# Performance work log

Measured on AMD Instinct MI355X. Metric: run time of the kernel, lower is better.

The kernel has to match this reference:

```python
import jax, jax.numpy as jnp
import numpy as np

BLOCK = 32  # GGUF Q8_0 block size: one scale per 32 int8 quants


def setup_inputs() -> dict:
    key = jax.random.key(0)
    k1, k2, k3, k4 = jax.random.split(key, 4)
    B, S, D_IN, D_OUT = 2, 2048, 4096, 16384
    x = jax.random.normal(k1, (B, S, D_IN), dtype=jnp.float32)
    # Stored quantized weights: unsigned byte codes in [0,255]; dequant as (q-128)*scale
    weight_q = jax.random.randint(k2, (D_OUT, D_IN), 0, 255, dtype=jnp.int32)
    # One positive scale per 32-element block along in_features
    scales = jax.random.uniform(k3, (D_OUT, D_IN // BLOCK), dtype=jnp.float32) * 0.02 + 1e-3
    bias = jax.random.normal(k4, (D_OUT,), dtype=jnp.float32)
    return {"x": x, "weight_q": weight_q, "scales": scales, "bias": bias}


def _dequant(weight_q, scales):
    # weight_q: [O, I] int codes, scales: [O, I/BLOCK] -> fp weight [O, I]
    O, I = weight_q.shape
    q = (weight_q.astype(jnp.float32) - 128.0).reshape(O, I // BLOCK, BLOCK)
    return (q * scales[:, :, None]).reshape(O, I)


def reference(x, weight_q, scales, bias):
    # Fused dequant + matmul: y = x @ dequant(W).T + bias
    w = _dequant(weight_q, scales)  # [O, I]
    y = jnp.einsum("bsi,oi->bso", x, w)
    return y + bias
```

## Files before the change

kernel.cpp:

```cpp
#include <hip/hip_runtime.h>
#include <hip/hip_bf16.h>

typedef __attribute__((ext_vector_type(8))) short short8;
typedef __attribute__((ext_vector_type(4))) float f32x4;

#define AS1 __attribute__((address_space(1)))
#define AS3 __attribute__((address_space(3)))

static __device__ __forceinline__ short f2bf(float f) {
    __hip_bfloat16 h = __float2bfloat16(f);
    union { __hip_bfloat16 h; short s; } u;
    u.h = h;
    return u.s;
}


__global__ __launch_bounds__(256) void prepack_w_kernel(const int* __restrict__ wq,
                                                        const float* __restrict__ scales,
                                                        short* __restrict__ Wb,
                                                        long total8) {
    long i = (long)blockIdx.x * 256 + threadIdx.x;
    if (i >= total8) return;
    const int4* p = (const int4*)wq + i * 2;
    int4 q0 = p[0], q1 = p[1];
    float s = scales[(i * 8) >> 5];
    short8 v;
    v[0] = f2bf((float)(q0.x - 128) * s);
    v[1] = f2bf((float)(q0.y - 128) * s);
    v[2] = f2bf((float)(q0.z - 128) * s);
    v[3] = f2bf((float)(q0.w - 128) * s);
    v[4] = f2bf((float)(q1.x - 128) * s);
    v[5] = f2bf((float)(q1.y - 128) * s);
    v[6] = f2bf((float)(q1.z - 128) * s);
    v[7] = f2bf((float)(q1.w - 128) * s);
    ((short8*)Wb)[i] = v;
}

__global__ __launch_bounds__(256) void prepack_x_kernel(const float* __restrict__ x,
                                                        short* __restrict__ Xb,
                                                        long total8) {
    long i = (long)blockIdx.x * 256 + threadIdx.x;
    if (i >= total8) return;
    const float4* p = (const float4*)x + i * 2;
    float4 f0 = p[0], f1 = p[1];
    short8 v;
    v[0] = f2bf(f0.x); v[1] = f2bf(f0.y); v[2] = f2bf(f0.z); v[3] = f2bf(f0.w);
    v[4] = f2bf(f1.x); v[5] = f2bf(f1.y); v[6] = f2bf(f1.z); v[7] = f2bf(f1.w);
    ((short8*)Xb)[i] = v;
}

__global__ __launch_bounds__(512, 2)
void gemm256_kernel(const float* __restrict__ bias,
                    const short* __restrict__ Xb, const short* __restrict__ Wb,
                    float* __restrict__ out, int M, int N, int K) {
    __shared__ alignas(16) short As[4 * 8192];
    __shared__ alignas(16) short Bs[4 * 8192];

    const int nM = M >> 8, nN = N >> 8;
    int bid = blockIdx.x;
    {
        int nwg = nM * nN;
        if ((nwg & 7) == 0) bid = (bid & 7) * (nwg >> 3) + (bid >> 3);
    }
    int pm, pn;
    {
        const int G = 8;
        if ((nN % G) == 0) {
            int per = nM * G;
            int grp = bid / per, in = bid % per;
            pn = grp * G + (in % G);
            pm = in / G;
        } else { pn = bid % nN; pm = bid / nN; }
    }

    const int tid  = threadIdx.x;
    const int lane = tid & 63;
    const int wid  = tid >> 6;
    const int wm   = wid >> 2;
    const int wn   = wid & 3;
    const int q4   = lane >> 4;
    const int l15  = lane & 15;
    const int lx   = lane & 7;

    const long bm = (long)pm << 8, bn = (long)pn << 8;
    const long Kl = K;
    const int  NT = K >> 6;

    int rdA[2], rdB[2];
#pragma unroll
    for (int p = 0; p < 2; ++p) {
        rdA[p] = (p * 2 + wm) * 8192 + l15 * 64;
        rdB[p] = (p * 2 + (wn >> 1)) * 8192 + ((wn & 1) * 64 + l15) * 64;
    }
    const int sg0 = ((0 * 4 + q4) ^ lx) * 8;
    const int sg1 = ((1 * 4 + q4) ^ lx) * 8;

    const int chnk    = wid * 1024;
    const int srowrel = wid * 16 + (lane >> 3);
    const int scol    = ((lane & 7) ^ (lane >> 3)) * 8;

    const short* aSrc[2][2];
    const short* bSrc[2][2];
#pragma unroll
    for (int H = 0; H < 2; ++H)
#pragma unroll
        for (int j = 0; j < 2; ++j) {
            aSrc[H][j] = Xb + (bm + H * 128 + srowrel + j * 8) * Kl + scol;
            bSrc[H][j] = Wb + (bn + H * 128 + srowrel + j * 8) * Kl + scol;
        }

#define STAGE_A(H, t1) { int p_ = (t1) & 1; long ko_ = (long)(t1) << 6;              \
    __builtin_amdgcn_global_load_lds((const AS1 void*)(aSrc[H][0] + ko_),            \
        (AS3 void*)&As[(p_ * 2 + (H)) * 8192 + chnk], 16, 0, 0);                     \
    __builtin_amdgcn_global_load_lds((const AS1 void*)(aSrc[H][1] + ko_),            \
        (AS3 void*)&As[(p_ * 2 + (H)) * 8192 + chnk + 512], 16, 0, 0); }
#define STAGE_B(H, t2) { int p_ = (t2) & 1; long ko_ = (long)(t2) << 6;              \
    __builtin_amdgcn_global_load_lds((const AS1 void*)(bSrc[H][0] + ko_),            \
        (AS3 void*)&Bs[(p_ * 2 + (H)) * 8192 + chnk], 16, 0, 0);                     \
    __builtin_amdgcn_global_load_lds((const AS1 void*)(bSrc[H][1] + ko_),            \
        (AS3 void*)&Bs[(p_ * 2 + (H)) * 8192 + chnk + 512], 16, 0, 0); }

    f32x4 acc[8][4];
#pragma unroll
    for (int m = 0; m < 8; ++m)
#pragma unroll
        for (int n = 0; n < 4; ++n) acc[m][n] = (f32x4){0.f, 0.f, 0.f, 0.f};

    short8 bfr[4][2];

    STAGE_B(0, 0); STAGE_B(1, 0);
    STAGE_A(0, 0); STAGE_A(1, 0);
    if (NT > 1) {
        STAGE_B(0, 1); STAGE_B(1, 1);
        asm volatile("s_waitcnt vmcnt(4)" ::: "memory");
    } else {
        asm volatile("s_waitcnt vmcnt(0)" ::: "memory");
    }
    __builtin_amdgcn_s_barrier();

    for (int t = 0; t < NT; ++t) {
        const int par = t & 1;
        const int ra = rdA[par], rb = rdB[par];
        const bool s1 = (t + 1 < NT), s2 = (t + 2 < NT);

#pragma unroll
        for (int q = 0; q < 4; ++q) {
            short8 ak[2][2];
#pragma unroll
            for (int mi = 0; mi < 2; ++mi) {
                ak[mi][0] = *(const short8*)&As[ra + (2 * q + mi) * 1024 + sg0];
                ak[mi][1] = *(const short8*)&As[ra + (2 * q + mi) * 1024 + sg1];
            }
            if (q == 0) {
#pragma unroll
                for (int n = 0; n < 4; ++n) {
                    bfr[n][0] = *(const short8*)&Bs[rb + n * 1024 + sg0];
                    bfr[n][1] = *(const short8*)&Bs[rb + n * 1024 + sg1];
                }
            }
            if (q == 0) { if (s1) STAGE_A(0, t + 1); }
            else if (q == 1) { if (s1) STAGE_A(1, t + 1); }
            else if (q == 2) { if (s2) STAGE_B(0, t + 2); }
            else           { if (s2) STAGE_B(1, t + 2); }

            if (q == 0) asm volatile("s_waitcnt lgkmcnt(8)" ::: "memory");
            __builtin_amdgcn_s_barrier();
            asm volatile("s_waitcnt lgkmcnt(0)" ::: "memory");
            __builtin_amdgcn_sched_barrier(0);

            __builtin_amdgcn_s_setprio(1);
#pragma unroll
            for (int mi = 0; mi < 2; ++mi) {
#pragma unroll
                for (int n = 0; n < 4; ++n)
                    acc[2 * q + mi][n] = __builtin_amdgcn_mfma_f32_16x16x32_bf16(
                        ak[mi][0], bfr[n][0], acc[2 * q + mi][n], 0, 0, 0);
#pragma unroll
                for (int n = 0; n < 4; ++n)
                    acc[2 * q + mi][n] = __builtin_amdgcn_mfma_f32_16x16x32_bf16(
                        ak[mi][1], bfr[n][1], acc[2 * q + mi][n], 0, 0, 0);
            }
            __builtin_amdgcn_s_setprio(0);

            if (q == 3) {
                if (s2)      asm volatile("s_waitcnt vmcnt(4)" ::: "memory");
                else if (s1) asm volatile("s_waitcnt vmcnt(0)" ::: "memory");
            }
            __builtin_amdgcn_s_barrier();
        }
        __builtin_amdgcn_sched_barrier(0);
    }

#pragma unroll
    for (int n = 0; n < 4; ++n) {
        long col = bn + wn * 64 + n * 16 + l15;
        float bv = bias[col];
#pragma unroll
        for (int m = 0; m < 8; ++m) {
            long row = bm + wm * 128 + m * 16 + q4 * 4;
#pragma unroll
            for (int r = 0; r < 4; ++r)
                out[(row + r) * (long)N + col] = acc[m][n][r] + bv;
        }
    }
#undef STAGE_A
#undef STAGE_B
}


template <bool PRE_A, bool PRE_B>
__global__ __launch_bounds__(256, 2)
void gemm_kernel(const float* __restrict__ x, const int* __restrict__ wq,
                 const float* __restrict__ scales, const float* __restrict__ bias,
                 const short* __restrict__ Xb, const short* __restrict__ Wb,
                 float* __restrict__ out, int M, int N, int K) {
    constexpr int BM = 128, BN = 128, BK = 64;
    __shared__ alignas(16) short As[BM * BK];
    __shared__ alignas(16) short Bs[BN * BK];

    const int nM = M / BM, nN = N / BN;
    int bid = blockIdx.x;
    int pm, pn;
    const int G = 8;
    if ((nN % G) == 0) {
        int per = nM * G;
        int grp = bid / per;
        int in  = bid % per;
        pn = grp * G + (in % G);
        pm = in / G;
    } else {
        pn = bid % nN;
        pm = bid / nN;
    }

    const int tid  = threadIdx.x;
    const int lane = tid & 63;
    const int wv   = tid >> 6;
    const int wm   = (wv >> 1) * 64;
    const int wn   = (wv & 1) * 64;
    const int q    = lane >> 4;
    const int l15  = lane & 15;
    const int sxor = lane & 7;

    const long bm = (long)pm * BM, bn = (long)pn * BN;

    f32x4 acc[4][4];
#pragma unroll
    for (int i = 0; i < 4; ++i)
#pragma unroll
        for (int j = 0; j < 4; ++j) acc[i][j] = (f32x4){0.f, 0.f, 0.f, 0.f};

    const int srow = tid >> 3;
    const int scg  = tid & 7;

    const int sg0   = q ^ sxor;
    const int aOff0 = (wm + l15) * 64 + sg0 * 8;
    const int aOff1 = (wm + l15) * 64 + (sg0 ^ 4) * 8;
    const int bOff0 = (wn + l15) * 64 + sg0 * 8;
    const int bOff1 = (wn + l15) * 64 + (sg0 ^ 4) * 8;

    const int prRow  = lane >> 3;
    const int prGsrc = (lane & 7) ^ (lane >> 3);

    for (int k0 = 0; k0 < K; k0 += BK) {
        if constexpr (PRE_A) {
#pragma unroll
            for (int i = 0; i < 4; ++i) {
                int r = wv * 32 + i * 8 + prRow;
                const short* src = Xb + (bm + r) * (long)K + k0 + prGsrc * 8;
                __builtin_amdgcn_global_load_lds((const AS1 void*)src,
                                                 (AS3 void*)&As[(wv * 32 + i * 8) * 64],
                                                 16, 0, 0);
            }
        } else {
#pragma unroll
            for (int i = 0; i < 4; ++i) {
                int r = i * 32 + srow;
                const float4* p = (const float4*)(x + (bm + r) * (long)K + k0 + scg * 8);
                float4 f0 = p[0], f1 = p[1];
                short8 v;
                v[0] = f2bf(f0.x); v[1] = f2bf(f0.y); v[2] = f2bf(f0.z); v[3] = f2bf(f0.w);
                v[4] = f2bf(f1.x); v[5] = f2bf(f1.y); v[6] = f2bf(f1.z); v[7] = f2bf(f1.w);
                int sg = scg ^ (r & 7);
                *(short8*)&As[r * 64 + sg * 8] = v;
            }
        }
        if constexpr (PRE_B) {
#pragma unroll
            for (int i = 0; i < 4; ++i) {
                int r = wv * 32 + i * 8 + prRow;
                const short* src = Wb + (bn + r) * (long)K + k0 + prGsrc * 8;
                __builtin_amdgcn_global_load_lds((const AS1 void*)src,
                                                 (AS3 void*)&Bs[(wv * 32 + i * 8) * 64],
                                                 16, 0, 0);
            }
        } else {
#pragma unroll
            for (int i = 0; i < 4; ++i) {
                int r = i * 32 + srow;
                const int4* p = (const int4*)(wq + (bn + r) * (long)K + k0 + scg * 8);
                int4 q0 = p[0], q1 = p[1];
                float s = scales[(bn + r) * (long)(K >> 5) + ((k0 + scg * 8) >> 5)];
                short8 v;
                v[0] = f2bf((float)(q0.x - 128) * s);
                v[1] = f2bf((float)(q0.y - 128) * s);
                v[2] = f2bf((float)(q0.z - 128) * s);
                v[3] = f2bf((float)(q0.w - 128) * s);
                v[4] = f2bf((float)(q1.x - 128) * s);
                v[5] = f2bf((float)(q1.y - 128) * s);
                v[6] = f2bf((float)(q1.z - 128) * s);
                v[7] = f2bf((float)(q1.w - 128) * s);
                int sg = scg ^ (r & 7);
                *(short8*)&Bs[r * 64 + sg * 8] = v;
            }
        }
        __syncthreads();

#pragma unroll
        for (int kk = 0; kk < 2; ++kk) {
            short8 a[4], b[4];
            const int aBase = kk ? aOff1 : aOff0;
            const int bBase = kk ? bOff1 : bOff0;
#pragma unroll
            for (int mi = 0; mi < 4; ++mi) a[mi] = *(const short8*)&As[aBase + mi * 16 * 64];
#pragma unroll
            for (int nj = 0; nj < 4; ++nj) b[nj] = *(const short8*)&Bs[bBase + nj * 16 * 64];
#pragma unroll
            for (int mi = 0; mi < 4; ++mi)
#pragma unroll
                for (int nj = 0; nj < 4; ++nj)
                    acc[mi][nj] = __builtin_amdgcn_mfma_f32_16x16x32_bf16(
                        a[mi], b[nj], acc[mi][nj], 0, 0, 0);
        }
        __syncthreads();
    }

#pragma unroll
    for (int nj = 0; nj < 4; ++nj) {
        long col = bn + wn + nj * 16 + l15;
        float bv = bias[col];
#pragma unroll
        for (int mi = 0; mi < 4; ++mi) {
            long row = bm + wm + mi * 16 + q * 4;
#pragma unroll
            for (int r2 = 0; r2 < 4; ++r2)
                out[(row + r2) * (long)N + col] = acc[mi][nj][r2] + bv;
        }
    }
}


extern "C" void kernel_launch(void* const* d_in, const int* in_sizes, int n_in,
                              void* d_out, int out_size, void* d_ws, size_t ws_size,
                              hipStream_t stream) {
    const float* x      = (const float*)d_in[0];
    const int*   wq     = (const int*)d_in[1];
    const float* scales = (const float*)d_in[2];
    const float* bias   = (const float*)d_in[3];
    float*       out    = (float*)d_out;

    const long N = (long)in_sizes[3];
    const long K = (long)in_sizes[1] / N;
    const long M = (long)in_sizes[0] / K;

    const size_t needW = (size_t)N * K * sizeof(short);
    const size_t needX = (size_t)M * K * sizeof(short);

    short* Wb = (short*)d_ws;
    short* Xb = Wb + (size_t)N * K;

    const bool preB = (d_ws != nullptr) && ws_size >= needW;
    const bool preA = preB && ws_size >= (needW + needX);

    if (preB) {
        long t8 = N * K / 8;
        prepack_w_kernel<<<dim3((unsigned)((t8 + 255) / 256)), dim3(256), 0, stream>>>(
            wq, scales, Wb, t8);
    }
    if (preA) {
        long t8 = M * K / 8;
        prepack_x_kernel<<<dim3((unsigned)((t8 + 255) / 256)), dim3(256), 0, stream>>>(
            x, Xb, t8);
    }

    const bool big = preA && (M % 256 == 0) && (N % 256 == 0) && (K % 64 == 0) && (K / 64 >= 2);

    if (big) {
        dim3 grid((unsigned)((M / 256) * (N / 256))), block(512);
        gemm256_kernel<<<grid, block, 0, stream>>>(bias, Xb, Wb, out, (int)M, (int)N, (int)K);
    } else {
        dim3 grid((unsigned)((M / 128) * (N / 128))), block(256);
        if (preA)
            gemm_kernel<true, true><<<grid, block, 0, stream>>>(x, wq, scales, bias, Xb, Wb,
                                                                out, (int)M, (int)N, (int)K);
        else if (preB)
            gemm_kernel<false, true><<<grid, block, 0, stream>>>(x, wq, scales, bias, Xb, Wb,
                                                                 out, (int)M, (int)N, (int)K);
        else
            gemm_kernel<false, false><<<grid, block, 0, stream>>>(x, wq, scales, bias, Xb, Wb,
                                                                  out, (int)M, (int)N, (int)K);
    }
}
```

Measured before the change: 645.1 us.

## Software-pipeline LDS fragment reads with ping-pong registers across MFMA phases

Restructures the main K loop of the 256x256 GEMM so that A fragments for the next phase are read from LDS into alternate register buffers (akP/akQ) while the current phase's MFMAs run. Next-tile B fragments are interleaved with the last MFMA phase. The last iteration is peeled into an epilogue. The aim is to hide LDS read latency behind matrix math and cut the full lgkmcnt(0) waits per phase, at the cost of more registers and a fragile hand-written wait schedule. It also drops the NT==1 guard in the prologue.

```diff
diff --git a/kernel.cpp b/kernel.cpp
--- a/kernel.cpp
+++ b/kernel.cpp
@@ -92,8 +92,8 @@
         rdA[p] = (p * 2 + wm) * 8192 + l15 * 64;
         rdB[p] = (p * 2 + (wn >> 1)) * 8192 + ((wn & 1) * 64 + l15) * 64;
     }
-    const int sg0 = ((0 * 4 + q4) ^ lx) * 8;
-    const int sg1 = ((1 * 4 + q4) ^ lx) * 8;
+    const int sg0 = (q4 ^ lx) * 8;
+    const int sg1 = ((4 + q4) ^ lx) * 8;
 
     const int chnk    = wid * 1024;
     const int srowrel = wid * 16 + (lane >> 3);
@@ -120,75 +120,122 @@
     __builtin_amdgcn_global_load_lds((const AS1 void*)(bSrc[H][1] + ko_),            \
         (AS3 void*)&Bs[(p_ * 2 + (H)) * 8192 + chnk + 512], 16, 0, 0); }
 
+#define LDA4(BUF, mbase, ra_) {                                                      \
+    BUF[0][0] = *(const short8*)&As[(ra_) + (mbase) * 1024 + sg0];                   \
+    BUF[0][1] = *(const short8*)&As[(ra_) + (mbase) * 1024 + sg1];                   \
+    BUF[1][0] = *(const short8*)&As[(ra_) + ((mbase) + 1) * 1024 + sg0];             \
+    BUF[1][1] = *(const short8*)&As[(ra_) + ((mbase) + 1) * 1024 + sg1]; }
+
+#define LGKM4  asm volatile("s_waitcnt lgkmcnt(4)" ::: "memory");                    \
+               __builtin_amdgcn_sched_barrier(0)
+#define LGKM0  asm volatile("s_waitcnt lgkmcnt(0)" ::: "memory");                    \
+               __builtin_amdgcn_sched_barrier(0)
+
+#define MFMA_PH(row0, A) {                                                           \
+    __builtin_amdgcn_s_setprio(1);                                                   \
+    _Pragma("unroll")                                                                \
+    for (int n = 0; n < 4; ++n)                                                      \
+        acc[row0][n] = __builtin_amdgcn_mfma_f32_16x16x32_bf16(A[0][0], bfr[n][0],   \
+                                                               acc[row0][n], 0,0,0); \
+    _Pragma("unroll")                                                                \
+    for (int n = 0; n < 4; ++n)                                                      \
+        acc[row0][n] = __builtin_amdgcn_mfma_f32_16x16x32_bf16(A[0][1], bfr[n][1],   \
+                                                               acc[row0][n], 0,0,0); \
+    _Pragma("unroll")                                                                \
+    for (int n = 0; n < 4; ++n)                                                      \
+        acc[(row0)+1][n] = __builtin_amdgcn_mfma_f32_16x16x32_bf16(A[1][0],          \
+                                           bfr[n][0], acc[(row0)+1][n], 0,0,0);      \
+    _Pragma("unroll")                                                                \
+    for (int n = 0; n < 4; ++n)                                                      \
+        acc[(row0)+1][n] = __builtin_amdgcn_mfma_f32_16x16x32_bf16(A[1][1],          \
+                                           bfr[n][1], acc[(row0)+1][n], 0,0,0);      \
+    __builtin_amdgcn_s_setprio(0); }
+
     f32x4 acc[8][4];
 #pragma unroll
     for (int m = 0; m < 8; ++m)
 #pragma unroll
         for (int n = 0; n < 4; ++n) acc[m][n] = (f32x4){0.f, 0.f, 0.f, 0.f};
 
-    short8 bfr[4][2];
-
-    STAGE_B(0, 0); STAGE_B(1, 0);
-    STAGE_A(0, 0); STAGE_A(1, 0);
-    if (NT > 1) {
-        STAGE_B(0, 1); STAGE_B(1, 1);
-        asm volatile("s_waitcnt vmcnt(4)" ::: "memory");
-    } else {
-        asm volatile("s_waitcnt vmcnt(0)" ::: "memory");
-    }
+    short8 akP[2][2], akQ[2][2], bfr[4][2];
+
+    STAGE_B(0, 0); STAGE_B(1, 0); STAGE_A(0, 0); STAGE_A(1, 0);
+    STAGE_B(0, 1); STAGE_B(1, 1);
+    asm volatile("s_waitcnt vmcnt(4)" ::: "memory");
     __builtin_amdgcn_s_barrier();
-
-    for (int t = 0; t < NT; ++t) {
+    LDA4(akP, 0, rdA[0]);
+#pragma unroll
+    for (int n = 0; n < 4; ++n) {
+        bfr[n][0] = *(const short8*)&Bs[rdB[0] + n * 1024 + sg0];
+        bfr[n][1] = *(const short8*)&Bs[rdB[0] + n * 1024 + sg1];
+    }
+
+    for (int t = 0; t < NT - 1; ++t) {
         const int par = t & 1;
-        const int ra = rdA[par], rb = rdB[par];
-        const bool s1 = (t + 1 < NT), s2 = (t + 2 < NT);
-
-#pragma unroll
-        for (int q = 0; q < 4; ++q) {
-            short8 ak[2][2];
-#pragma unroll
-            for (int mi = 0; mi < 2; ++mi) {
-                ak[mi][0] = *(const short8*)&As[ra + (2 * q + mi) * 1024 + sg0];
-                ak[mi][1] = *(const short8*)&As[ra + (2 * q + mi) * 1024 + sg1];
-            }
-            if (q == 0) {
-#pragma unroll
-                for (int n = 0; n < 4; ++n) {
-                    bfr[n][0] = *(const short8*)&Bs[rb + n * 1024 + sg0];
-                    bfr[n][1] = *(const short8*)&Bs[rb + n * 1024 + sg1];
-                }
-            }
-            if (q == 0) { if (s1) STAGE_A(0, t + 1); }
-            else if (q == 1) { if (s1) STAGE_A(1, t + 1); }
-            else if (q == 2) { if (s2) STAGE_B(0, t + 2); }
-            else           { if (s2) STAGE_B(1, t + 2); }
-
-            if (q == 0) asm volatile("s_waitcnt lgkmcnt(8)" ::: "memory");
-            __builtin_amdgcn_s_barrier();
-            asm volatile("s_waitcnt lgkmcnt(0)" ::: "memory");
-            __builtin_amdgcn_sched_barrier(0);
-
-            __builtin_amdgcn_s_setprio(1);
-#pragma unroll
-            for (int mi = 0; mi < 2; ++mi) {
-#pragma unroll
-                for (int n = 0; n < 4; ++n)
-                    acc[2 * q + mi][n] = __builtin_amdgcn_mfma_f32_16x16x32_bf16(
-                        ak[mi][0], bfr[n][0], acc[2 * q + mi][n], 0, 0, 0);
-#pragma unroll
-                for (int n = 0; n < 4; ++n)
-                    acc[2 * q + mi][n] = __builtin_amdgcn_mfma_f32_16x16x32_bf16(
-                        ak[mi][1], bfr[n][1], acc[2 * q + mi][n], 0, 0, 0);
-            }
-            __builtin_amdgcn_s_setprio(0);
-
-            if (q == 3) {
-                if (s2)      asm volatile("s_waitcnt vmcnt(4)" ::: "memory");
-                else if (s1) asm volatile("s_waitcnt vmcnt(0)" ::: "memory");
-            }
-            __builtin_amdgcn_s_barrier();
-        }
-        __builtin_amdgcn_sched_barrier(0);
+        const int ra = rdA[par], ran = rdA[par ^ 1], rbn = rdB[par ^ 1];
+        const bool s2 = (t + 2 < NT);
+
+        LDA4(akQ, 2, ra);
+        STAGE_A(0, t + 1);
+        LGKM4;
+        MFMA_PH(0, akP);
+        __builtin_amdgcn_s_barrier();
+        LDA4(akP, 4, ra);
+        STAGE_A(1, t + 1);
+        LGKM4;
+        MFMA_PH(2, akQ);
+        __builtin_amdgcn_s_barrier();
+        LDA4(akQ, 6, ra);
+        if (s2) STAGE_B(0, t + 2);
+        LGKM4;
+        MFMA_PH(4, akP);
+        __builtin_amdgcn_s_barrier();
+        if (s2) { asm volatile("s_waitcnt vmcnt(2)" ::: "memory"); }
+        else    { asm volatile("s_waitcnt vmcnt(0)" ::: "memory"); }
+        __builtin_amdgcn_s_barrier();
+        LDA4(akP, 0, ran);
+        if (s2) STAGE_B(1, t + 2);
+        LGKM4;
+        __builtin_amdgcn_s_setprio(1);
+#pragma unroll
+        for (int n = 0; n < 4; ++n)
+            acc[6][n] = __builtin_amdgcn_mfma_f32_16x16x32_bf16(akQ[0][0], bfr[n][0],
+                                                                acc[6][n], 0, 0, 0);
+#pragma unroll
+        for (int n = 0; n < 4; ++n)
+            acc[6][n] = __builtin_amdgcn_mfma_f32_16x16x32_bf16(akQ[0][1], bfr[n][1],
+                                                                acc[6][n], 0, 0, 0);
+#pragma unroll
+        for (int n = 0; n < 4; ++n) {
+            acc[7][n] = __builtin_amdgcn_mfma_f32_16x16x32_bf16(akQ[1][0], bfr[n][0],
+                                                                acc[7][n], 0, 0, 0);
+            bfr[n][0] = *(const short8*)&Bs[rbn + n * 1024 + sg0];
+        }
+#pragma unroll
+        for (int n = 0; n < 4; ++n) {
+            acc[7][n] = __builtin_amdgcn_mfma_f32_16x16x32_bf16(akQ[1][1], bfr[n][1],
+                                                                acc[7][n], 0, 0, 0);
+            bfr[n][1] = *(const short8*)&Bs[rbn + n * 1024 + sg1];
+        }
+        __builtin_amdgcn_s_setprio(0);
+        __builtin_amdgcn_s_barrier();
+    }
+
+    {
+        const int ra = rdA[(NT - 1) & 1];
+        LDA4(akQ, 2, ra);
+        LGKM4;
+        MFMA_PH(0, akP);
+        __builtin_amdgcn_s_barrier();
+        LDA4(akP, 4, ra);
+        LGKM4;
+        MFMA_PH(2, akQ);
+        __builtin_amdgcn_s_barrier();
+        LDA4(akQ, 6, ra);
+        LGKM4;
+        MFMA_PH(4, akP);
+        LGKM0;
+        MFMA_PH(6, akQ);
     }
 
 #pragma unroll
@@ -205,6 +252,10 @@
     }
 #undef STAGE_A
 #undef STAGE_B
+#undef LDA4
+#undef LGKM4
+#undef LGKM0
+#undef MFMA_PH
 }
 
 
```

After: 649.3 us. About the same (+0.6%).
